# Kernel tuning notes

Hardware: AMD Instinct MI355X
Metric: run time of the kernel (lower is better)

Reference implementation:

```python
import jax, jax.numpy as jnp
import numpy as np

K = 20
DEPTH = 4
EMB = 1024
NEG = 0.2   # LeakyReLU slope
EPS = 1e-5  # BatchNorm eps (inference mode: running_mean=0, running_var=1)


def _bn_lrelu(x, g, b):
    # inference BatchNorm over channel axis 1 with mean=0, var=1, then LeakyReLU(0.2)
    sh = [1] * x.ndim
    sh[1] = -1
    y = x * (g / jnp.sqrt(1.0 + EPS)).reshape(sh) + b.reshape(sh)
    return jnp.where(y >= 0, y, NEG * y)


def _attention_edge(x, Wq, Wk, Wv):
    # x: (G, N, C). Full self-attention, topk neighbor selection, EdgeConv features.
    C = x.shape[-1]
    q = x @ Wq.T
    k = x @ Wk.T
    v = x @ Wv.T
    att = jax.nn.softmax(jnp.einsum('gnc,gmc->gnm', q, k) / jnp.sqrt(jnp.float32(C)), axis=-1)
    out = jnp.einsum('gnm,gmc->gnc', att, v)
    idx = jax.lax.top_k(att, K)[1]                      # (G,N,K) neighbor indices
    xt = x + out                                        # residual: x + x_sa
    feat = jax.vmap(lambda a, i: a[i])(xt, idx)         # (G,N,K,C) gather
    ctr = jnp.broadcast_to(xt[:, :, None, :], feat.shape)
    return jnp.concatenate([feat - ctr, ctr], axis=-1)  # (G,N,K,2C)


def _seq_graph_feature(x, Wq, Wk, Wv):
    # x: (B, F, C, N) -> (B, 2C, F, N, K); vectorizes the per-sample Python loop
    B, F, C, N = x.shape
    xf = x.reshape(B * F, C, N).transpose(0, 2, 1)      # (G,N,C)
    e = _attention_edge(xf, Wq, Wk, Wv)                 # (G,N,K,2C)
    return e.reshape(B, F, N, K, 2 * C).transpose(0, 4, 1, 2, 3)


def setup_inputs() -> dict:
    key = jax.random.key(0)
    ks = jax.random.split(key, 16)
    d = {}
    d['x'] = jax.random.normal(ks[0], (8, 32, 3, 512), jnp.float32)
    d['Wq1'] = jax.random.normal(ks[1], (3, 3), jnp.float32) * 0.5
    d['Wk1'] = jax.random.normal(ks[2], (3, 3), jnp.float32) * 0.5
    d['Wv1'] = jax.random.normal(ks[3], (3, 3), jnp.float32) * 0.5
    d['Wq2'] = jax.random.normal(ks[4], (64, 64), jnp.float32) * 0.1
    d['Wk2'] = jax.random.normal(ks[5], (64, 64), jnp.float32) * 0.1
    d['Wv2'] = jax.random.normal(ks[6], (64, 64), jnp.float32) * 0.1
    d['conv1_w'] = jax.random.normal(ks[7], (64, 6, DEPTH, 3, 3), jnp.float32) * 0.1
    d['conv2_w'] = jax.random.normal(ks[8], (128, 128), jnp.float32) * 0.05
    d['conv5_w'] = jax.random.normal(ks[9], (EMB, 192), jnp.float32) * 0.05
    d['bn1_g'] = jax.random.uniform(ks[10], (64,), jnp.float32, 0.5, 1.5)
    d['bn1_b'] = jax.random.normal(ks[11], (64,), jnp.float32) * 0.1
    d['bn2_g'] = jax.random.uniform(ks[12], (128,), jnp.float32, 0.5, 1.5)
    d['bn2_b'] = jax.random.normal(ks[13], (128,), jnp.float32) * 0.1
    d['bn5_g'] = jax.random.uniform(ks[14], (EMB,), jnp.float32, 0.5, 1.5)
    d['bn5_b'] = jax.random.normal(ks[15], (EMB,), jnp.float32) * 0.1
    return d


def reference(x, Wq1, Wk1, Wv1, Wq2, Wk2, Wv2, conv1_w, conv2_w, conv5_w,
              bn1_g, bn1_b, bn2_g, bn2_b, bn5_g, bn5_b):
    y = _seq_graph_feature(x, Wq1, Wk1, Wv1)                      # (B,6,F,N,K)
    y = jax.lax.conv_general_dilated(
        y, conv1_w, window_strides=(DEPTH, 2, 1), padding='VALID',
        dimension_numbers=('NCDHW', 'OIDHW', 'NCDHW'))            # (B,64,F',N',K-2)
    y = _bn_lrelu(y, bn1_g, bn1_b)
    x1 = y.max(axis=-1)                                           # (B,64,F',N')
    x1p = x1.transpose(0, 2, 1, 3)                                # (B,F',64,N')
    y = _seq_graph_feature(x1p, Wq2, Wk2, Wv2)                    # (B,128,F',N',K)
    y = jnp.einsum('bcfnk,oc->bofnk', y, conv2_w)                 # 1x1x1 conv3d
    y = _bn_lrelu(y, bn2_g, bn2_b)
    x2 = y.max(axis=-1)                                           # (B,128,F',N')
    y = jnp.concatenate([x1, x2], axis=1)                         # (B,192,F',N')
    y = jnp.einsum('bcfn,oc->bofn', y, conv5_w)                   # 1x1 conv2d
    y = _bn_lrelu(y, bn5_g, bn5_b)
    emb = y.max(axis=-1).transpose(0, 2, 1)                       # (B,F',EMB)
    return emb
```

## Files before the change

kernel.cpp:

```cpp
#include <hip/hip_runtime.h>
#include <hip/hip_bf16.h>
#include <math.h>

typedef float f4 __attribute__((ext_vector_type(4)));

#define NEG 0.2f
#define BN_EPS 1e-5f

#define CE(K,A,B) { unsigned long long _x = K[A], _y = K[B]; bool _s = _x < _y; \
                    K[A] = _s ? _y : _x; K[B] = _s ? _x : _y; }

__device__ __forceinline__ float wred_max_f32(float v) {
  int x = __float_as_int(v), y;
#define STEPM(C) y = __builtin_amdgcn_update_dpp(x, x, C, 0xf, 0xf, false); \
  x = __float_as_int(fmaxf(__int_as_float(x), __int_as_float(y)));
  STEPM(0x111) STEPM(0x112) STEPM(0x114) STEPM(0x118) STEPM(0x142) STEPM(0x143)
#undef STEPM
  return __int_as_float(__builtin_amdgcn_readlane(x, 63));
}
__device__ __forceinline__ float wred_sum_f32(float v) {
  int x = __float_as_int(v), y;
#define STEPS(C) y = __builtin_amdgcn_update_dpp(0, x, C, 0xf, 0xf, true); \
  x = __float_as_int(__int_as_float(x) + __int_as_float(y));
  STEPS(0x111) STEPS(0x112) STEPS(0x114) STEPS(0x118) STEPS(0x142) STEPS(0x143)
#undef STEPS
  return __int_as_float(__builtin_amdgcn_readlane(x, 63));
}
__device__ __forceinline__ unsigned wred16_max_u32(unsigned v) {
  int x = (int)v, y;
#define STEPU(C) y = __builtin_amdgcn_update_dpp(x, x, C, 0xf, 0xf, false); \
  x = (int)((unsigned)x > (unsigned)y ? (unsigned)x : (unsigned)y);
  STEPU(0x111) STEPU(0x112) STEPU(0x114) STEPU(0x118)
#undef STEPU
  unsigned a0 = (unsigned)__builtin_amdgcn_readlane(x, 15);
  unsigned a1 = (unsigned)__builtin_amdgcn_readlane(x, 31);
  unsigned a2 = (unsigned)__builtin_amdgcn_readlane(x, 47);
  unsigned a3 = (unsigned)__builtin_amdgcn_readlane(x, 63);
  unsigned m01 = a0 > a1 ? a0 : a1;
  unsigned m23 = a2 > a3 ? a2 : a3;
  return m01 > m23 ? m01 : m23;
}

__device__ __forceinline__ unsigned sel_round8(unsigned (&hi)[8], unsigned (&lo)[8],
                                               bool do_pop) {
  unsigned gv = wred16_max_u32(hi[0]);
  unsigned long long tied = __ballot(hi[0] == gv);
  unsigned gl;
  if (__popcll(tied) == 1) {
    int wl = __ffsll((long long)tied) - 1;
    gl = (unsigned)__builtin_amdgcn_readlane((int)lo[0], wl);
  } else {
    gl = wred16_max_u32((hi[0] == gv) ? lo[0] : 0u);
  }
  if (do_pop) {
    bool win = (hi[0] == gv) && (lo[0] == gl);
    hi[0] = win ? hi[1] : hi[0]; lo[0] = win ? lo[1] : lo[0];
    hi[1] = win ? hi[2] : hi[1]; lo[1] = win ? lo[2] : lo[1];
    hi[2] = win ? hi[3] : hi[2]; lo[2] = win ? lo[3] : lo[2];
    hi[3] = win ? hi[4] : hi[3]; lo[3] = win ? lo[4] : lo[3];
    hi[4] = win ? hi[5] : hi[4]; lo[4] = win ? lo[5] : lo[4];
    hi[5] = win ? hi[6] : hi[5]; lo[5] = win ? lo[6] : lo[5];
    hi[6] = win ? hi[7] : hi[6]; lo[6] = win ? lo[7] : lo[6];
    hi[7] = win ? 0u    : hi[7]; lo[7] = win ? 0u    : lo[7];
  }
  return gl;
}
__device__ __forceinline__ unsigned sel_round4(unsigned (&hi)[4], unsigned (&lo)[4],
                                               bool do_pop) {
  unsigned gv = wred16_max_u32(hi[0]);
  unsigned long long tied = __ballot(hi[0] == gv);
  unsigned gl;
  if (__popcll(tied) == 1) {
    int wl = __ffsll((long long)tied) - 1;
    gl = (unsigned)__builtin_amdgcn_readlane((int)lo[0], wl);
  } else {
    gl = wred16_max_u32((hi[0] == gv) ? lo[0] : 0u);
  }
  if (do_pop) {
    bool win = (hi[0] == gv) && (lo[0] == gl);
    hi[0] = win ? hi[1] : hi[0]; lo[0] = win ? lo[1] : lo[0];
    hi[1] = win ? hi[2] : hi[1]; lo[1] = win ? lo[2] : lo[1];
    hi[2] = win ? hi[3] : hi[2]; lo[2] = win ? lo[3] : lo[2];
    hi[3] = win ? 0u    : hi[3]; lo[3] = win ? 0u    : lo[3];
  }
  return gl;
}

__global__ __launch_bounds__(256) void qkv1_k(const float* __restrict__ x,
    const float* __restrict__ Wk, const float* __restrict__ Wv,
    float* __restrict__ k1, float* __restrict__ v1) {
#pragma clang fp contract(off)
  int g = blockIdx.y;
  int n = blockIdx.x * 256 + threadIdx.x;
  const float* xr = x + (size_t)g * 1536;
  float x0 = xr[n], x1v = xr[512 + n], x2v = xr[1024 + n];
  f4 kd, vd;
#pragma unroll
  for (int o = 0; o < 3; ++o) {
    kd[o] = x0 * Wk[o*3+0] + x1v * Wk[o*3+1] + x2v * Wk[o*3+2];
    vd[o] = x0 * Wv[o*3+0] + x1v * Wv[o*3+1] + x2v * Wv[o*3+2];
  }
  kd[3] = 0.f; vd[3] = 0.f;
  *(f4*)(k1 + ((size_t)g * 512 + n) * 4) = kd;
  *(f4*)(v1 + ((size_t)g * 512 + n) * 4) = vd;
}

__global__ __launch_bounds__(256) void attn1_k(const float* __restrict__ x,
    const float* __restrict__ Wq, const float* __restrict__ k1,
    const float* __restrict__ v1, float* __restrict__ xt1p, int* __restrict__ idx1) {
  __shared__ f4 kl[512];
  __shared__ f4 vl[512];
  int t = threadIdx.x, g = blockIdx.y;
  int w = t >> 6, l = t & 63;
  int nb = blockIdx.x * 16;
  const f4* kgp = (const f4*)(k1 + (size_t)g * 2048);
  const f4* vgp = (const f4*)(v1 + (size_t)g * 2048);
  for (int i = t; i < 512; i += 256) { kl[i] = kgp[i]; vl[i] = vgp[i]; }
  __syncthreads();
  const float* xr = x + (size_t)g * 1536;
  for (int rp = 0; rp < 2; ++rp) {
    int nA = nb + rp * 8 + w;
    int nB = nA + 4;
    float xA0 = xr[nA], xA1 = xr[512 + nA], xA2 = xr[1024 + nA];
    float xB0 = xr[nB], xB1 = xr[512 + nB], xB2 = xr[1024 + nB];
    float qA0, qA1, qA2, qB0, qB1, qB2;
    float aA[8], aB[8];
    {
#pragma clang fp contract(off)
      qA0 = xA0*Wq[0] + xA1*Wq[1] + xA2*Wq[2];
      qA1 = xA0*Wq[3] + xA1*Wq[4] + xA2*Wq[5];
      qA2 = xA0*Wq[6] + xA1*Wq[7] + xA2*Wq[8];
      qB0 = xB0*Wq[0] + xB1*Wq[1] + xB2*Wq[2];
      qB1 = xB0*Wq[3] + xB1*Wq[4] + xB2*Wq[5];
      qB2 = xB0*Wq[6] + xB1*Wq[7] + xB2*Wq[8];
#pragma unroll
      for (int j = 0; j < 8; ++j) {
        f4 kk = kl[l + 64 * j];
        aA[j] = (qA0*kk[0] + qA1*kk[1] + qA2*kk[2]) / sqrtf(3.0f);
        aB[j] = (qB0*kk[0] + qB1*kk[1] + qB2*kk[2]) / sqrtf(3.0f);
      }
    }
    float mxA = aA[0], mxB = aB[0];
#pragma unroll
    for (int j = 1; j < 8; ++j) { mxA = fmaxf(mxA, aA[j]); mxB = fmaxf(mxB, aB[j]); }
    mxA = wred_max_f32(mxA); mxB = wred_max_f32(mxB);
    float wsA = 0.f, wsB = 0.f;
#pragma unroll
    for (int j = 0; j < 8; ++j) {
      aA[j] = expf(aA[j] - mxA); wsA += aA[j];
      aB[j] = expf(aB[j] - mxB); wsB += aB[j];
    }
    wsA = wred_sum_f32(wsA); wsB = wred_sum_f32(wsB);
#pragma unroll
    for (int j = 0; j < 8; ++j) { aA[j] = aA[j] / wsA; aB[j] = aB[j] / wsB; }
    float oA0 = 0.f, oA1 = 0.f, oA2 = 0.f, oB0 = 0.f, oB1 = 0.f, oB2 = 0.f;
#pragma unroll
    for (int j = 0; j < 8; ++j) {
      f4 vv = vl[l + 64 * j];
      oA0 += aA[j] * vv[0]; oA1 += aA[j] * vv[1]; oA2 += aA[j] * vv[2];
      oB0 += aB[j] * vv[0]; oB1 += aB[j] * vv[1]; oB2 += aB[j] * vv[2];
    }
    oA0 = wred_sum_f32(oA0); oA1 = wred_sum_f32(oA1); oA2 = wred_sum_f32(oA2);
    oB0 = wred_sum_f32(oB0); oB1 = wred_sum_f32(oB1); oB2 = wred_sum_f32(oB2);
    if (l == 0) {
      float* xo = xt1p + ((size_t)g * 512 + nA) * 4;
      xo[0] = xA0 + oA0; xo[1] = xA1 + oA1; xo[2] = xA2 + oA2;
      float* xo2 = xt1p + ((size_t)g * 512 + nB) * 4;
      xo2[0] = xB0 + oB0; xo2[1] = xB1 + oB1; xo2[2] = xB2 + oB2;
    }
    unsigned long long keyA[8], keyB[8];
#pragma unroll
    for (int j = 0; j < 8; ++j) {
      unsigned idx = (unsigned)(l + 64 * j);
      keyA[j] = ((unsigned long long)__float_as_uint(aA[j]) << 32) | (unsigned)(~idx);
      keyB[j] = ((unsigned long long)__float_as_uint(aB[j]) << 32) | (unsigned)(~idx);
    }
    CE(keyA,0,1) CE(keyA,2,3) CE(keyA,4,5) CE(keyA,6,7)
    CE(keyA,0,2) CE(keyA,1,3) CE(keyA,4,6) CE(keyA,5,7)
    CE(keyA,1,2) CE(keyA,5,6)
    CE(keyA,0,4) CE(keyA,1,5) CE(keyA,2,6) CE(keyA,3,7)
    CE(keyA,2,4) CE(keyA,3,5)
    CE(keyA,1,2) CE(keyA,3,4) CE(keyA,5,6)
    CE(keyB,0,1) CE(keyB,2,3) CE(keyB,4,5) CE(keyB,6,7)
    CE(keyB,0,2) CE(keyB,1,3) CE(keyB,4,6) CE(keyB,5,7)
    CE(keyB,1,2) CE(keyB,5,6)
    CE(keyB,0,4) CE(keyB,1,5) CE(keyB,2,6) CE(keyB,3,7)
    CE(keyB,2,4) CE(keyB,3,5)
    CE(keyB,1,2) CE(keyB,3,4) CE(keyB,5,6)
    unsigned hiA[8], loA[8], hiB[8], loB[8];
#pragma unroll
    for (int j = 0; j < 8; ++j) {
      hiA[j] = (unsigned)(keyA[j] >> 32); loA[j] = (unsigned)keyA[j];
      hiB[j] = (unsigned)(keyB[j] >> 32); loB[j] = (unsigned)keyB[j];
    }
    int* ioA = idx1 + ((size_t)g * 512 + nA) * 20;
    int* ioB = idx1 + ((size_t)g * 512 + nB) * 20;
    for (int kk = 0; kk < 20; ++kk) {
      unsigned gA = sel_round8(hiA, loA, kk < 19);
      unsigned gB = sel_round8(hiB, loB, kk < 19);
      if (l == 0) { ioA[kk] = (int)(~gA); ioB[kk] = (int)(~gB); }
    }
  }
}

__global__ __launch_bounds__(256) void conv1_k(const float* __restrict__ xt1p,
    const int* __restrict__ idx1, const float* __restrict__ w1,
    const float* __restrict__ bg, const float* __restrict__ bb,
    float* __restrict__ x1g) {
  __shared__ float wt[108][64];
  __shared__ float cwt[36][64];
  __shared__ __align__(16) float yfl[4][10][3][20];
  __shared__ float ycl[4][10][4];
  int t = threadIdx.x;
  int fp = blockIdx.y, b = blockIdx.z;
  int np0 = blockIdx.x * 16;
  int o = t & 63, part = t >> 6;
  for (int i = part; i < 108; i += 4) {
    int w3 = i % 3, rh = i / 3;
    int cc = rh / 12, dh = rh % 12;
    wt[i][o] = w1[o * 216 + cc * 36 + dh * 3 + w3];
  }
  for (int i = part; i < 36; i += 4) {
    int cc = i / 12, dh = i % 12;
    const float* ww = &w1[o * 216 + (cc + 3) * 36 + dh * 3];
    cwt[i][o] = ww[0] + ww[1] + ww[2];
  }
  int g2 = b * 8 + fp;
  for (int rnd = 0; rnd < 4; ++rnd) {
    int npr = np0 + rnd * 4;
    __syncthreads();
    for (int it = t; it < 800; it += 256) {
      int d = it / 200, rem = it % 200, nl = rem / 20, k = rem % 20;
      int n = 2 * npr + nl;
      if (n < 512) {
        int g = b * 32 + fp * 4 + d;
        int j = idx1[((size_t)g * 512 + n) * 20 + k];
        f4 vj = *(const f4*)(xt1p + ((size_t)g * 512 + j) * 4);
        f4 vc = *(const f4*)(xt1p + ((size_t)g * 512 + n) * 4);
        yfl[d][nl][0][k] = vj[0] - vc[0];
        yfl[d][nl][1][k] = vj[1] - vc[1];
        yfl[d][nl][2][k] = vj[2] - vc[2];
      } else {
        yfl[d][nl][0][k] = 0.f; yfl[d][nl][1][k] = 0.f; yfl[d][nl][2][k] = 0.f;
      }
    }
    if (t < 40) {
      int d = t / 10, nl = t % 10;
      int n = 2 * npr + nl;
      if (n < 512) {
        int g = b * 32 + fp * 4 + d;
        f4 vc = *(const f4*)(xt1p + ((size_t)g * 512 + n) * 4);
        ycl[d][nl][0] = vc[0]; ycl[d][nl][1] = vc[1]; ycl[d][nl][2] = vc[2];
      } else {
        ycl[d][nl][0] = 0.f; ycl[d][nl][1] = 0.f; ycl[d][nl][2] = 0.f;
      }
    }
    __syncthreads();
    int np = npr + part;
    if (np < 255) {
      float fa[18] = {0.f,0.f,0.f,0.f,0.f,0.f,0.f,0.f,0.f,
                      0.f,0.f,0.f,0.f,0.f,0.f,0.f,0.f,0.f};
      float ctr = 0.f;
      for (int cc = 0; cc < 3; ++cc) {
        for (int dh = 0; dh < 12; ++dh) {
          int d = dh / 3, h = dh % 3;
          int nl = 2 * part + h;
          int ib = (cc * 12 + dh) * 3;
          float w0 = wt[ib][o], w1v = wt[ib + 1][o], w2v = wt[ib + 2][o];
          ctr += ycl[d][nl][cc] * cwt[cc * 12 + dh][o];
          const f4* yr = (const f4*)&yfl[d][nl][cc][0];
          float y[20];
#pragma unroll
          for (int q = 0; q < 5; ++q) {
            f4 v = yr[q];
            y[4*q+0] = v[0]; y[4*q+1] = v[1]; y[4*q+2] = v[2]; y[4*q+3] = v[3];
          }
#pragma unroll
          for (int kp = 0; kp < 18; ++kp)
            fa[kp] += w0 * y[kp] + w1v * y[kp + 1] + w2v * y[kp + 2];
        }
      }
      float vmax = fa[0];
#pragma unroll
      for (int kp = 1; kp < 18; ++kp) vmax = fmaxf(vmax, fa[kp]);
      vmax += ctr;
      float sc = bg[o] / sqrtf(1.0f + BN_EPS);
      float z = sc * vmax + bb[o];
      if (z < 0.f) z *= NEG;
      x1g[((size_t)g2 * 255 + np) * 64 + o] = z;
    }
  }
}

__global__ __launch_bounds__(256) void qkv2_k(const float* __restrict__ x1g,
    const float* __restrict__ Wq, const float* __restrict__ Wk, const float* __restrict__ Wv,
    float* __restrict__ q2, float* __restrict__ k2, float* __restrict__ v2) {
  __shared__ float Wl[3][64 * 65];
  __shared__ float rowl[4][64];
  int t = threadIdx.x, g = blockIdx.y;
  int w = t >> 6, l = t & 63;
  for (int i = t; i < 4096; i += 256) {
    int r = i >> 6, c = i & 63;
    Wl[0][r * 65 + c] = Wq[i];
    Wl[1][r * 65 + c] = Wk[i];
    Wl[2][r * 65 + c] = Wv[i];
  }
  __syncthreads();
  for (int rr = 0; rr < 8; ++rr) {
    int n = blockIdx.x * 32 + rr * 4 + w;
    bool valid = n < 255;
    rowl[w][l] = valid ? x1g[((size_t)g * 255 + n) * 64 + l] : 0.f;
    float qa = 0.f, ka = 0.f, va = 0.f;
    for (int c = 0; c < 64; ++c) {
      float rv = rowl[w][c];
      qa += rv * Wl[0][l * 65 + c];
      ka += rv * Wl[1][l * 65 + c];
      va += rv * Wl[2][l * 65 + c];
    }
    if (valid) {
      size_t off = ((size_t)g * 255 + n) * 64 + l;
      q2[off] = qa; k2[off] = ka; v2[off] = va;
    }
  }
}

__global__ __launch_bounds__(256) void attn2_k(const float* __restrict__ q2,
    const float* __restrict__ k2, const float* __restrict__ v2,
    const float* __restrict__ x1g, float* __restrict__ xt2, int* __restrict__ idx2) {
  __shared__ __align__(16) float Kl[255 * 64];
  __shared__ __align__(16) float Vl[255 * 64];
  __shared__ __align__(16) float pl[4][4][256];
  __shared__ __align__(16) float ql[4][4][64];
  int t = threadIdx.x, g = blockIdx.y;
  int w = t >> 6, l = t & 63;
  int n0 = blockIdx.x * 64;
  const float* kg = k2 + (size_t)g * 16320;
  const float* vg = v2 + (size_t)g * 16320;
  for (int i = t; i < 4080; i += 256) {
    int m = i >> 4, c4 = (i & 15) << 2;
    f4 kv = *(const f4*)(kg + (size_t)i * 4);
    f4 vv = *(const f4*)(vg + (size_t)i * 4);
    *(f4*)&Kl[m * 64 + (c4 ^ ((m & 7) << 2))] = kv;
    *(f4*)&Vl[m * 64 + c4] = vv;
  }
  __syncthreads();
  for (int grp = 0; grp < 4; ++grp) {
    int rbase = n0 + w * 16 + grp * 4;
#pragma unroll
    for (int r = 0; r < 4; ++r) {
      int n = rbase + r;
      ql[w][r][l] = (n < 255) ? q2[((size_t)g * 255 + n) * 64 + l] : 0.f;
    }
    float s[4][4] = {};
    for (int c4 = 0; c4 < 64; c4 += 4) {
      f4 kv[4];
#pragma unroll
      for (int j = 0; j < 4; ++j) {
        int m = l + 64 * j;
        kv[j] = *(const f4*)&Kl[m * 64 + (c4 ^ ((m & 7) << 2))];
      }
#pragma unroll
      for (int r = 0; r < 4; ++r) {
        f4 qv = *(const f4*)&ql[w][r][c4];
#pragma unroll
        for (int j = 0; j < 4; ++j)
          s[r][j] += qv[0]*kv[j][0] + qv[1]*kv[j][1] + qv[2]*kv[j][2] + qv[3]*kv[j][3];
      }
    }
    unsigned Hi[4][4], Lo[4][4];
#pragma unroll
    for (int r = 0; r < 4; ++r) {
#pragma unroll
      for (int j = 0; j < 4; ++j) s[r][j] = s[r][j] / 8.0f;
      if (l == 63) s[r][3] = -1e30f;
      float mx = fmaxf(fmaxf(s[r][0], s[r][1]), fmaxf(s[r][2], s[r][3]));
      mx = wred_max_f32(mx);
      float ws = 0.f;
#pragma unroll
      for (int j = 0; j < 4; ++j) { s[r][j] = expf(s[r][j] - mx); ws += s[r][j]; }
      ws = wred_sum_f32(ws);
      unsigned long long key[4];
#pragma unroll
      for (int j = 0; j < 4; ++j) {
        s[r][j] = s[r][j] / ws;
        pl[w][r][64 * j + l] = s[r][j];
        key[j] = ((unsigned long long)__float_as_uint(s[r][j]) << 32)
               | (unsigned)(~(unsigned)(64 * j + l));
      }
      CE(key,0,1) CE(key,2,3) CE(key,0,2) CE(key,1,3) CE(key,1,2)
#pragma unroll
      for (int j = 0; j < 4; ++j) {
        Hi[r][j] = (unsigned)(key[j] >> 32); Lo[r][j] = (unsigned)key[j];
      }
    }
    float acc[4] = {0.f, 0.f, 0.f, 0.f};
    for (int m4 = 0; m4 < 256; m4 += 4) {
      f4 pv[4];
#pragma unroll
      for (int r = 0; r < 4; ++r) pv[r] = *(const f4*)&pl[w][r][m4];
      float v0 = Vl[(m4 + 0) * 64 + l];
      float v1 = Vl[(m4 + 1) * 64 + l];
      float v2v = Vl[(m4 + 2) * 64 + l];
      float v3 = Vl[(m4 + 3) * 64 + l];
#pragma unroll
      for (int r = 0; r < 4; ++r)
        acc[r] += pv[r][0]*v0 + pv[r][1]*v1 + pv[r][2]*v2v + pv[r][3]*v3;
    }
#pragma unroll
    for (int r = 0; r < 4; ++r) {
      int n = rbase + r;
      if (n < 255) {
        size_t off = ((size_t)g * 255 + n) * 64 + l;
        xt2[off] = x1g[off] + acc[r];
      }
    }
    int* io0 = idx2 + ((size_t)g * 255 + rbase + 0) * 20;
    int* io1 = idx2 + ((size_t)g * 255 + rbase + 1) * 20;
    int* io2 = idx2 + ((size_t)g * 255 + rbase + 2) * 20;
    int* io3 = idx2 + ((size_t)g * 255 + rbase + 3) * 20;
    for (int kk = 0; kk < 20; ++kk) {
      unsigned g0 = sel_round4(Hi[0], Lo[0], kk < 19);
      unsigned g1 = sel_round4(Hi[1], Lo[1], kk < 19);
      unsigned g2v = sel_round4(Hi[2], Lo[2], kk < 19);
      unsigned g3 = sel_round4(Hi[3], Lo[3], kk < 19);
      if (l == 0) {
        if (rbase + 0 < 255) io0[kk] = (int)(~g0);
        if (rbase + 1 < 255) io1[kk] = (int)(~g1);
        if (rbase + 2 < 255) io2[kk] = (int)(~g2v);
        if (rbase + 3 < 255) io3[kk] = (int)(~g3);
      }
    }
  }
}

__global__ __launch_bounds__(256) void conv2_k(const float* __restrict__ xt2,
    const int* __restrict__ idx2, const float* __restrict__ w2,
    const float* __restrict__ bg, const float* __restrict__ bb,
    float* __restrict__ x2g) {
  __shared__ __align__(16) float w2h[64 * 128];
  __shared__ float rows[8][21][64];
  int t = threadIdx.x, g = blockIdx.y;
  int n0 = blockIdx.x * 8;
  for (int i = t; i < 10752; i += 256) {
    int pos = i / 1344, rem = i % 1344, r = rem >> 6, c = rem & 63;
    int n = n0 + pos;
    float v = 0.f;
    if (n < 255) {
      if (r < 20) {
        int j = idx2[((size_t)g * 255 + n) * 20 + r];
        v = xt2[((size_t)g * 255 + j) * 64 + c];
      } else v = xt2[((size_t)g * 255 + n) * 64 + c];
    }
    rows[pos][r][c] = v;
  }
  for (int i = t; i < 8192; i += 256) {
    int o2 = i >> 6, c = i & 63;
    w2h[c * 128 + (o2 ^ (c & 28))] = w2[o2 * 128 + c];
  }
  __syncthreads();
  int os = t & 31, np = t >> 5;
  float acc[4][20] = {};
  float t1[4] = {0.f, 0.f, 0.f, 0.f};
  for (int c = 0; c < 64; ++c) {
    f4 wq = *(const f4*)&w2h[c * 128 + ((os * 4) ^ (c & 28))];
    float cv = rows[np][20][c];
#pragma unroll
    for (int i = 0; i < 4; ++i) t1[i] += wq[i] * cv;
#pragma unroll
    for (int j = 0; j < 20; ++j) {
      float rv = rows[np][j][c];
#pragma unroll
      for (int i = 0; i < 4; ++i) acc[i][j] += wq[i] * rv;
    }
  }
  __syncthreads();
  for (int i = t; i < 8192; i += 256) {
    int o2 = i >> 6, c = i & 63;
    w2h[c * 128 + (o2 ^ (c & 28))] = w2[o2 * 128 + 64 + c];
  }
  __syncthreads();
  float t2[4] = {0.f, 0.f, 0.f, 0.f};
  for (int c = 0; c < 64; ++c) {
    f4 wq = *(const f4*)&w2h[c * 128 + ((os * 4) ^ (c & 28))];
    float cv = rows[np][20][c];
#pragma unroll
    for (int i = 0; i < 4; ++i) t2[i] += wq[i] * cv;
  }
  int n = n0 + np;
  f4 res;
#pragma unroll
  for (int i = 0; i < 4; ++i) {
    float vm = -1e30f;
#pragma unroll
    for (int j = 0; j < 20; ++j) vm = fmaxf(vm, acc[i][j]);
    vm += t2[i] - t1[i];
    int o = os * 4 + i;
    float sc = bg[o] / sqrtf(1.0f + BN_EPS);
    float z = sc * vm + bb[o];
    if (z < 0.f) z *= NEG;
    res[i] = z;
  }
  if (n < 255)
    *(f4*)&x2g[((size_t)g * 255 + n) * 128 + os * 4] = res;
}

__global__ __launch_bounds__(256) void conv5_k(const float* __restrict__ x1g,
    const float* __restrict__ x2g, const float* __restrict__ w5,
    const float* __restrict__ bg, const float* __restrict__ bb,
    float* __restrict__ out) {
  __shared__ __align__(16) float w5h[96 * 64];
  __shared__ float colh[32][97];
  __shared__ float red[16][64];
  int t = threadIdx.x;
  int ot = blockIdx.x, fp = blockIdx.y, b = blockIdx.z;
  size_t rowbase = ((size_t)b * 8 + fp) * 255;
  int os = t & 15, ns = t >> 4;
  float vm[4] = {-1e30f, -1e30f, -1e30f, -1e30f};
  for (int gh = 0; gh < 2; ++gh) {
    float acc[4][4][2] = {};
    for (int ch = 0; ch < 2; ++ch) {
      __syncthreads();
      for (int i = t; i < 6144; i += 256) {
        int oL = i / 96, c = i % 96;
        w5h[c * 64 + (oL ^ (c & 28))] = w5[((size_t)(ot * 64 + oL)) * 192 + ch * 96 + c];
      }
#pragma unroll
      for (int gl = 0; gl < 4; ++gl) {
        int grp = gh * 4 + gl;
        __syncthreads();
        for (int i = t; i < 3072; i += 256) {
          int nl = i / 96, c = i % 96;
          int n = grp * 32 + nl;
          float v = 0.f;
          if (n < 255) {
            int cc = ch * 96 + c;
            v = (cc < 64) ? x1g[(rowbase + n) * 64 + cc]
                          : x2g[(rowbase + n) * 128 + (cc - 64)];
          }
          colh[nl][c] = v;
        }
        __syncthreads();
        for (int c = 0; c < 96; ++c) {
          f4 wq = *(const f4*)&w5h[c * 64 + ((os * 4) ^ (c & 28))];
#pragma unroll
          for (int vv = 0; vv < 2; ++vv) {
            float cvv = colh[ns * 2 + vv][c];
#pragma unroll
            for (int u = 0; u < 4; ++u) acc[gl][u][vv] += wq[u] * cvv;
          }
        }
      }
    }
#pragma unroll
    for (int gl = 0; gl < 4; ++gl)
#pragma unroll
      for (int vv = 0; vv < 2; ++vv) {
        int n = (gh * 4 + gl) * 32 + ns * 2 + vv;
        if (n < 255)
#pragma unroll
          for (int u = 0; u < 4; ++u) vm[u] = fmaxf(vm[u], acc[gl][u][vv]);
      }
  }
#pragma unroll
  for (int u = 0; u < 4; ++u) red[ns][os * 4 + u] = vm[u];
  __syncthreads();
  if (t < 64) {
    float m = -1e30f;
#pragma unroll
    for (int q = 0; q < 16; ++q) m = fmaxf(m, red[q][t]);
    int o = ot * 64 + t;
    float sc = bg[o] / sqrtf(1.0f + BN_EPS);
    float z = sc * m + bb[o];
    if (z < 0.f) z *= NEG;
    out[((size_t)b * 8 + fp) * 1024 + o] = z;
  }
}

extern "C" void kernel_launch(void* const* d_in, const int* in_sizes, int n_in,
                              void* d_out, int out_size, void* d_ws, size_t ws_size,
                              hipStream_t stream) {
  const float* x   = (const float*)d_in[0];
  const float* Wq1 = (const float*)d_in[1];
  const float* Wk1 = (const float*)d_in[2];
  const float* Wv1 = (const float*)d_in[3];
  const float* Wq2 = (const float*)d_in[4];
  const float* Wk2 = (const float*)d_in[5];
  const float* Wv2 = (const float*)d_in[6];
  const float* w1  = (const float*)d_in[7];
  const float* w2  = (const float*)d_in[8];
  const float* w5  = (const float*)d_in[9];
  const float* bg1 = (const float*)d_in[10];
  const float* bb1 = (const float*)d_in[11];
  const float* bg2 = (const float*)d_in[12];
  const float* bb2 = (const float*)d_in[13];
  const float* bg5 = (const float*)d_in[14];
  const float* bb5 = (const float*)d_in[15];
  float* out = (float*)d_out;
  float* ws  = (float*)d_ws;

  float* k1   = ws;
  float* v1   = ws + 524288;
  float* x1g  = ws;
  float* xt1p = ws + 1048576;
  int*   idx1 = (int*)(ws + 1572864);
  float* q2   = ws + 4194304;
  float* k2   = ws + 5238784;
  float* v2   = ws + 6283264;
  float* xt2  = ws + 7327744;
  int*   idx2 = (int*)(ws + 8372224);
  float* x2g  = ws + 8698624;

  qkv1_k<<<dim3(2, 256), 256, 0, stream>>>(x, Wk1, Wv1, k1, v1);
  attn1_k<<<dim3(32, 256), 256, 0, stream>>>(x, Wq1, k1, v1, xt1p, idx1);
  conv1_k<<<dim3(16, 8, 8), 256, 0, stream>>>(xt1p, idx1, w1, bg1, bb1, x1g);
  qkv2_k<<<dim3(8, 64), 256, 0, stream>>>(x1g, Wq2, Wk2, Wv2, q2, k2, v2);
  attn2_k<<<dim3(4, 64), 256, 0, stream>>>(q2, k2, v2, x1g, xt2, idx2);
  conv2_k<<<dim3(32, 64), 256, 0, stream>>>(xt2, idx2, w2, bg2, bb2, x2g);
  conv5_k<<<dim3(16, 8, 8), 256, 0, stream>>>(x1g, x2g, w5, bg5, bb5, out);
}
```

Baseline: 876.5 us.

## Fuse qkv1 into attn1 and transpose shared tiles in conv2/conv5 for vector reads

Stage-1 key/value projection is now computed inside attn1_k directly into shared memory, which removes the qkv1_k launch and its global round trip. The projection is recomputed by each of the 32 blocks per group. conv2_k stores the gathered neighbor rows transposed ([c][k]) with a separate center array, so the inner loop reads them as float4. conv5_k processes 64 points per group in a transposed [c][n] tile, giving each thread a 4x4 register block read with float4 loads. The cost is more accumulator registers and fewer reloads of the tile.

```diff
diff --git a/kernel.cpp b/kernel.cpp
--- a/kernel.cpp
+++ b/kernel.cpp
@@ -86,38 +86,30 @@
   return gl;
 }
 
-__global__ __launch_bounds__(256) void qkv1_k(const float* __restrict__ x,
-    const float* __restrict__ Wk, const float* __restrict__ Wv,
-    float* __restrict__ k1, float* __restrict__ v1) {
-#pragma clang fp contract(off)
-  int g = blockIdx.y;
-  int n = blockIdx.x * 256 + threadIdx.x;
-  const float* xr = x + (size_t)g * 1536;
-  float x0 = xr[n], x1v = xr[512 + n], x2v = xr[1024 + n];
-  f4 kd, vd;
-#pragma unroll
-  for (int o = 0; o < 3; ++o) {
-    kd[o] = x0 * Wk[o*3+0] + x1v * Wk[o*3+1] + x2v * Wk[o*3+2];
-    vd[o] = x0 * Wv[o*3+0] + x1v * Wv[o*3+1] + x2v * Wv[o*3+2];
-  }
-  kd[3] = 0.f; vd[3] = 0.f;
-  *(f4*)(k1 + ((size_t)g * 512 + n) * 4) = kd;
-  *(f4*)(v1 + ((size_t)g * 512 + n) * 4) = vd;
-}
-
 __global__ __launch_bounds__(256) void attn1_k(const float* __restrict__ x,
-    const float* __restrict__ Wq, const float* __restrict__ k1,
-    const float* __restrict__ v1, float* __restrict__ xt1p, int* __restrict__ idx1) {
+    const float* __restrict__ Wq, const float* __restrict__ Wk,
+    const float* __restrict__ Wv, float* __restrict__ xt1p, int* __restrict__ idx1) {
   __shared__ f4 kl[512];
   __shared__ f4 vl[512];
   int t = threadIdx.x, g = blockIdx.y;
   int w = t >> 6, l = t & 63;
   int nb = blockIdx.x * 16;
-  const f4* kgp = (const f4*)(k1 + (size_t)g * 2048);
-  const f4* vgp = (const f4*)(v1 + (size_t)g * 2048);
-  for (int i = t; i < 512; i += 256) { kl[i] = kgp[i]; vl[i] = vgp[i]; }
+  const float* xr = x + (size_t)g * 1536;
+  {
+#pragma clang fp contract(off)
+    for (int i = t; i < 512; i += 256) {
+      float x0 = xr[i], x1v = xr[512 + i], x2v = xr[1024 + i];
+      f4 kd, vd;
+#pragma unroll
+      for (int o = 0; o < 3; ++o) {
+        kd[o] = x0 * Wk[o*3+0] + x1v * Wk[o*3+1] + x2v * Wk[o*3+2];
+        vd[o] = x0 * Wv[o*3+0] + x1v * Wv[o*3+1] + x2v * Wv[o*3+2];
+      }
+      kd[3] = 0.f; vd[3] = 0.f;
+      kl[i] = kd; vl[i] = vd;
+    }
+  }
   __syncthreads();
-  const float* xr = x + (size_t)g * 1536;
   for (int rp = 0; rp < 2; ++rp) {
     int nA = nb + rp * 8 + w;
     int nB = nA + 4;
@@ -438,20 +430,24 @@
     const float* __restrict__ bg, const float* __restrict__ bb,
     float* __restrict__ x2g) {
   __shared__ __align__(16) float w2h[64 * 128];
-  __shared__ float rows[8][21][64];
+  __shared__ __align__(16) float rowsT[8][64][20];
+  __shared__ float ctr2[8][64];
   int t = threadIdx.x, g = blockIdx.y;
   int n0 = blockIdx.x * 8;
-  for (int i = t; i < 10752; i += 256) {
-    int pos = i / 1344, rem = i % 1344, r = rem >> 6, c = rem & 63;
+  for (int i = t; i < 10240; i += 256) {
+    int pos = i / 1280, rem = i % 1280, k = rem >> 6, c = rem & 63;
     int n = n0 + pos;
     float v = 0.f;
     if (n < 255) {
-      if (r < 20) {
-        int j = idx2[((size_t)g * 255 + n) * 20 + r];
-        v = xt2[((size_t)g * 255 + j) * 64 + c];
-      } else v = xt2[((size_t)g * 255 + n) * 64 + c];
-    }
-    rows[pos][r][c] = v;
+      int j = idx2[((size_t)g * 255 + n) * 20 + k];
+      v = xt2[((size_t)g * 255 + j) * 64 + c];
+    }
+    rowsT[pos][c][k] = v;
+  }
+  for (int i = t; i < 512; i += 256) {
+    int pos = i >> 6, c = i & 63;
+    int n = n0 + pos;
+    ctr2[pos][c] = (n < 255) ? xt2[((size_t)g * 255 + n) * 64 + c] : 0.f;
   }
   for (int i = t; i < 8192; i += 256) {
     int o2 = i >> 6, c = i & 63;
@@ -463,14 +459,16 @@
   float t1[4] = {0.f, 0.f, 0.f, 0.f};
   for (int c = 0; c < 64; ++c) {
     f4 wq = *(const f4*)&w2h[c * 128 + ((os * 4) ^ (c & 28))];
-    float cv = rows[np][20][c];
+    float cv = ctr2[np][c];
 #pragma unroll
     for (int i = 0; i < 4; ++i) t1[i] += wq[i] * cv;
 #pragma unroll
-    for (int j = 0; j < 20; ++j) {
-      float rv = rows[np][j][c];
-#pragma unroll
-      for (int i = 0; i < 4; ++i) acc[i][j] += wq[i] * rv;
+    for (int q = 0; q < 5; ++q) {
+      f4 rv = *(const f4*)&rowsT[np][c][4 * q];
+#pragma unroll
+      for (int e = 0; e < 4; ++e)
+#pragma unroll
+        for (int i = 0; i < 4; ++i) acc[i][4 * q + e] += wq[i] * rv[e];
     }
   }
   __syncthreads();
@@ -482,7 +480,7 @@
   float t2[4] = {0.f, 0.f, 0.f, 0.f};
   for (int c = 0; c < 64; ++c) {
     f4 wq = *(const f4*)&w2h[c * 128 + ((os * 4) ^ (c & 28))];
-    float cv = rows[np][20][c];
+    float cv = ctr2[np][c];
 #pragma unroll
     for (int i = 0; i < 4; ++i) t2[i] += wq[i] * cv;
   }
@@ -509,58 +507,54 @@
     const float* __restrict__ bg, const float* __restrict__ bb,
     float* __restrict__ out) {
   __shared__ __align__(16) float w5h[96 * 64];
-  __shared__ float colh[32][97];
+  __shared__ __align__(16) float colhT[96][68];
   __shared__ float red[16][64];
   int t = threadIdx.x;
   int ot = blockIdx.x, fp = blockIdx.y, b = blockIdx.z;
   size_t rowbase = ((size_t)b * 8 + fp) * 255;
   int os = t & 15, ns = t >> 4;
-  float vm[4] = {-1e30f, -1e30f, -1e30f, -1e30f};
-  for (int gh = 0; gh < 2; ++gh) {
-    float acc[4][4][2] = {};
-    for (int ch = 0; ch < 2; ++ch) {
+  float acc[4][4][4] = {};
+  for (int ch = 0; ch < 2; ++ch) {
+    __syncthreads();
+    for (int i = t; i < 6144; i += 256) {
+      int oL = i / 96, c = i % 96;
+      w5h[c * 64 + (oL ^ (c & 28))] = w5[((size_t)(ot * 64 + oL)) * 192 + ch * 96 + c];
+    }
+#pragma unroll
+    for (int grp = 0; grp < 4; ++grp) {
       __syncthreads();
       for (int i = t; i < 6144; i += 256) {
-        int oL = i / 96, c = i % 96;
-        w5h[c * 64 + (oL ^ (c & 28))] = w5[((size_t)(ot * 64 + oL)) * 192 + ch * 96 + c];
-      }
-#pragma unroll
-      for (int gl = 0; gl < 4; ++gl) {
-        int grp = gh * 4 + gl;
-        __syncthreads();
-        for (int i = t; i < 3072; i += 256) {
-          int nl = i / 96, c = i % 96;
-          int n = grp * 32 + nl;
-          float v = 0.f;
-          if (n < 255) {
-            int cc = ch * 96 + c;
-            v = (cc < 64) ? x1g[(rowbase + n) * 64 + cc]
-                          : x2g[(rowbase + n) * 128 + (cc - 64)];
-          }
-          colh[nl][c] = v;
+        int nl = i / 96, c = i % 96;
+        int n = grp * 64 + nl;
+        float v = 0.f;
+        if (n < 255) {
+          int cc = ch * 96 + c;
+          v = (cc < 64) ? x1g[(rowbase + n) * 64 + cc]
+                        : x2g[(rowbase + n) * 128 + (cc - 64)];
         }
-        __syncthreads();
-        for (int c = 0; c < 96; ++c) {
-          f4 wq = *(const f4*)&w5h[c * 64 + ((os * 4) ^ (c & 28))];
-#pragma unroll
-          for (int vv = 0; vv < 2; ++vv) {
-            float cvv = colh[ns * 2 + vv][c];
-#pragma unroll
-            for (int u = 0; u < 4; ++u) acc[gl][u][vv] += wq[u] * cvv;
-          }
-        }
-      }
-    }
-#pragma unroll
-    for (int gl = 0; gl < 4; ++gl)
-#pragma unroll
-      for (int vv = 0; vv < 2; ++vv) {
-        int n = (gh * 4 + gl) * 32 + ns * 2 + vv;
-        if (n < 255)
-#pragma unroll
-          for (int u = 0; u < 4; ++u) vm[u] = fmaxf(vm[u], acc[gl][u][vv]);
-      }
-  }
+        colhT[c][nl] = v;
+      }
+      __syncthreads();
+      for (int c = 0; c < 96; ++c) {
+        f4 wq = *(const f4*)&w5h[c * 64 + ((os * 4) ^ (c & 28))];
+        f4 cv = *(const f4*)&colhT[c][ns * 4];
+#pragma unroll
+        for (int u = 0; u < 4; ++u)
+#pragma unroll
+          for (int vv = 0; vv < 4; ++vv) acc[grp][u][vv] += wq[u] * cv[vv];
+      }
+    }
+  }
+  float vm[4] = {-1e30f, -1e30f, -1e30f, -1e30f};
+#pragma unroll
+  for (int grp = 0; grp < 4; ++grp)
+#pragma unroll
+    for (int vv = 0; vv < 4; ++vv) {
+      int n = grp * 64 + ns * 4 + vv;
+      if (n < 255)
+#pragma unroll
+        for (int u = 0; u < 4; ++u) vm[u] = fmaxf(vm[u], acc[grp][u][vv]);
+    }
 #pragma unroll
   for (int u = 0; u < 4; ++u) red[ns][os * 4 + u] = vm[u];
   __syncthreads();
@@ -598,8 +592,6 @@
   float* out = (float*)d_out;
   float* ws  = (float*)d_ws;
 
-  float* k1   = ws;
-  float* v1   = ws + 524288;
   float* x1g  = ws;
   float* xt1p = ws + 1048576;
   int*   idx1 = (int*)(ws + 1572864);
@@ -610,8 +602,7 @@
   int*   idx2 = (int*)(ws + 8372224);
   float* x2g  = ws + 8698624;
 
-  qkv1_k<<<dim3(2, 256), 256, 0, stream>>>(x, Wk1, Wv1, k1, v1);
-  attn1_k<<<dim3(32, 256), 256, 0, stream>>>(x, Wq1, k1, v1, xt1p, idx1);
+  attn1_k<<<dim3(32, 256), 256, 0, stream>>>(x, Wq1, Wk1, Wv1, xt1p, idx1);
   conv1_k<<<dim3(16, 8, 8), 256, 0, stream>>>(xt1p, idx1, w1, bg1, bb1, x1g);
   qkv2_k<<<dim3(8, 64), 256, 0, stream>>>(x1g, Wq2, Wk2, Wv2, q2, k2, v2);
   attn2_k<<<dim3(4, 64), 256, 0, stream>>>(q2, k2, v2, x1g, xt2, idx2);
```

Result: faster. 827.5 us (-5.6%).
